# Performance work log

Hardware: AMD Instinct MI355X
Metric: run time of the kernel (lower is better)

Reference implementation:

```python
import jax, jax.numpy as jnp
import numpy as np

N = 80000        # nodes
E = 1280000      # edges
NG = 8           # graphs (segment ids)
F_IN = 3
NC = 20
BN_EPS = 1e-3    # keras BatchNormalization default epsilon


def setup_inputs() -> dict:
    key = jax.random.key(0)
    ks = jax.random.split(key, 16)
    inp = {}
    inp['x'] = jax.random.normal(ks[0], (N, F_IN), dtype=jnp.float32)
    inp['edge_w'] = jax.random.uniform(ks[1], (E,), dtype=jnp.float32)
    inp['src'] = jax.random.randint(ks[2], (E,), 0, N, dtype=jnp.int32)
    inp['dst'] = jax.random.randint(ks[3], (E,), 0, N, dtype=jnp.int32)
    inp['ids'] = jnp.sort(jax.random.randint(ks[4], (N,), 0, NG, dtype=jnp.int32))
    def w(k, fi, fo):
        return jax.random.normal(k, (fi, fo), dtype=jnp.float32) * (1.0 / np.sqrt(fi))
    inp['W1'] = w(ks[5], F_IN, 32); inp['b1'] = jnp.zeros((32,), jnp.float32)
    inp['W2'] = w(ks[6], 32, 32);   inp['b2'] = jnp.zeros((32,), jnp.float32)
    inp['g1'] = jnp.ones((32,), jnp.float32); inp['be1'] = jnp.zeros((32,), jnp.float32)
    inp['m1'] = jax.random.normal(ks[7], (32,), dtype=jnp.float32) * 0.1
    inp['v1'] = jax.random.uniform(ks[8], (32,), dtype=jnp.float32) + 0.5
    inp['W3'] = w(ks[9], 32, 64);   inp['b3'] = jnp.zeros((64,), jnp.float32)
    inp['W4'] = w(ks[10], 64, 64);  inp['b4'] = jnp.zeros((64,), jnp.float32)
    inp['g2'] = jnp.ones((64,), jnp.float32); inp['be2'] = jnp.zeros((64,), jnp.float32)
    inp['m2'] = jax.random.normal(ks[11], (64,), dtype=jnp.float32) * 0.1
    inp['v2'] = jax.random.uniform(ks[12], (64,), dtype=jnp.float32) + 0.5
    inp['W5'] = w(ks[13], 64, NC);  inp['b5'] = jnp.zeros((NC,), jnp.float32)
    return inp


def _gcn(x, W, b, src, dst, ew):
    # Spektral GCNConv: A_norm @ (X W) + b, with A given as edge list (src->dst).
    h = x @ W                                      # [N, Fo] dense transform first (cheaper)
    msg = h[src] * ew[:, None]                     # gather + scale  [E, Fo]
    agg = jax.ops.segment_sum(msg, dst, num_segments=N)  # scatter-add [N, Fo]
    return agg + b


def _bn(x, g, be, m, v):
    # inference-mode BatchNormalization
    return (x - m) * (g * jax.lax.rsqrt(v + BN_EPS)) + be


def _pool(x, ids):
    # per-graph global max pooling, broadcast back to nodes
    mx = jax.ops.segment_max(x, ids, num_segments=NG)   # [NG, F]
    return mx[ids]                                       # [N, F]


def reference(x, edge_w, src, dst, ids,
              W1, b1, W2, b2, g1, be1, m1, v1,
              W3, b3, W4, b4, g2, be2, m2, v2,
              W5, b5):
    h = jax.nn.relu(_gcn(x, W1, b1, src, dst, edge_w))
    h = jax.nn.relu(_gcn(h, W2, b2, src, dst, edge_w))
    h = _bn(h, g1, be1, m1, v1)
    h = _pool(h, ids)
    h = jax.nn.relu(_gcn(h, W3, b3, src, dst, edge_w))
    h = jax.nn.relu(_gcn(h, W4, b4, src, dst, edge_w))
    h = _bn(h, g2, be2, m2, v2)
    h = _pool(h, ids)
    # dropout is identity in inference
    out = jax.nn.softmax(_gcn(h, W5, b5, src, dst, edge_w), axis=-1)
    return out
```

## Files before the change

### kernel.cpp

```cpp
#include <hip/hip_runtime.h>

#define NN 80000
#define NE 1280000
#define NGR 8
#define BN_EPS 1e-3f
#define NBF 625
#define GB 512
#define CHK 2500

typedef unsigned short ushort;
typedef __attribute__((ext_vector_type(8))) short bf16x8;
typedef __attribute__((ext_vector_type(4))) float f32x4;

__device__ __forceinline__ unsigned enc_f(float f) {
    unsigned b = __float_as_uint(f);
    return (f >= 0.f) ? (b | 0x80000000u) : ~b;
}
__device__ __forceinline__ float dec_f(unsigned u) {
    return (u & 0x80000000u) ? __uint_as_float(u & 0x7FFFFFFFu) : __uint_as_float(~u);
}
__device__ __forceinline__ ushort f2bf(float f) {
    unsigned u = __float_as_uint(f);
    unsigned r = u + 0x7FFFu + ((u >> 16) & 1u);
    return (ushort)(r >> 16);
}
__device__ __forceinline__ void fma8(float* acc, const ushort* p, float w) {
    uint4 q = *(const uint4*)p;
    acc[0] += w * __uint_as_float((q.x & 0xFFFFu) << 16);
    acc[1] += w * __uint_as_float(q.x & 0xFFFF0000u);
    acc[2] += w * __uint_as_float((q.y & 0xFFFFu) << 16);
    acc[3] += w * __uint_as_float(q.y & 0xFFFF0000u);
    acc[4] += w * __uint_as_float((q.z & 0xFFFFu) << 16);
    acc[5] += w * __uint_as_float(q.z & 0xFFFF0000u);
    acc[6] += w * __uint_as_float((q.w & 0xFFFFu) << 16);
    acc[7] += w * __uint_as_float(q.w & 0xFFFF0000u);
}

__global__ __launch_bounds__(256) void k_bhist(const int* __restrict__ dst,
                                               int* __restrict__ hcnt) {
    __shared__ int lh[NBF];
    for (int i = threadIdx.x; i < NBF; i += 256) lh[i] = 0;
    __syncthreads();
    int e0 = blockIdx.x * CHK;
    for (int e = e0 + threadIdx.x; e < e0 + CHK; e += 256)
        atomicAdd(&lh[dst[e] >> 7], 1);
    __syncthreads();
    int* row = hcnt + (size_t)blockIdx.x * NBF;
    for (int i = threadIdx.x; i < NBF; i += 256) row[i] = lh[i];
}

__global__ __launch_bounds__(256) void k_bbase1(int* __restrict__ hcnt,
                                                int* __restrict__ tot) {
    __shared__ int sm[256];
    int bin = blockIdx.x, t = threadIdx.x;
    int v[2];
    int s = 0;
    #pragma unroll
    for (int j = 0; j < 2; ++j) {
        v[j] = hcnt[(size_t)(t * 2 + j) * NBF + bin];
        s += v[j];
    }
    sm[t] = s;
    __syncthreads();
    #pragma unroll
    for (int off = 1; off < 256; off <<= 1) {
        int u = (t >= off) ? sm[t - off] : 0;
        __syncthreads();
        sm[t] += u;
        __syncthreads();
    }
    int run = sm[t] - s;
    if (t == 255) tot[bin] = sm[255];
    #pragma unroll
    for (int j = 0; j < 2; ++j) {
        hcnt[(size_t)(t * 2 + j) * NBF + bin] = run;
        run += v[j];
    }
}

__global__ __launch_bounds__(1024) void k_bbase2w(const int* __restrict__ tot,
                                                  int* __restrict__ bo,
                                                  const float* __restrict__ W2,
                                                  const float* __restrict__ W4,
                                                  ushort* __restrict__ W2t,
                                                  ushort* __restrict__ W4t) {
    __shared__ int sm[1024];
    int t = threadIdx.x;
    int v = (t < NBF) ? tot[t] : 0;
    sm[t] = v;
    __syncthreads();
    #pragma unroll
    for (int off = 1; off < 1024; off <<= 1) {
        int u = (t >= off) ? sm[t - off] : 0;
        __syncthreads();
        sm[t] += u;
        __syncthreads();
    }
    if (t < NBF) bo[t] = sm[t] - v;
    if (t == 0) bo[NBF] = NE;
    {
        int f = t >> 5, k = t & 31;
        W2t[t] = f2bf(W2[k * 32 + f]);
    }
    #pragma unroll
    for (int j = 0; j < 4; ++j) {
        int i = t + j * 1024;
        int f = i >> 6, k = i & 63;
        W4t[i] = f2bf(W4[k * 64 + f]);
    }
}

__global__ __launch_bounds__(256) void k_bfill(const int* __restrict__ src,
                                               const int* __restrict__ dst,
                                               const float* __restrict__ ew,
                                               const int* __restrict__ ids,
                                               const int* __restrict__ hcnt,
                                               const int* __restrict__ bo,
                                               int2* __restrict__ cB) {
    __shared__ int lh[NBF];
    __shared__ int delta[NBF];
    __shared__ int lcur[NBF];
    __shared__ int2 srt[CHK];
    __shared__ short sbin[CHK];
    __shared__ int sm[256];
    int t = threadIdx.x;
    int e0 = blockIdx.x * CHK;
    const int* row = hcnt + (size_t)blockIdx.x * NBF;
    for (int i = t; i < NBF; i += 256) lh[i] = 0;
    __syncthreads();
    for (int e = e0 + t; e < e0 + CHK; e += 256)
        atomicAdd(&lh[dst[e] >> 7], 1);
    __syncthreads();
    int c0, c1, c2;
    {
        int i0 = t * 3, i1 = t * 3 + 1, i2 = t * 3 + 2;
        c0 = (i0 < NBF) ? lh[i0] : 0;
        c1 = (i1 < NBF) ? lh[i1] : 0;
        c2 = (i2 < NBF) ? lh[i2] : 0;
    }
    int ssum = c0 + c1 + c2;
    sm[t] = ssum;
    __syncthreads();
    #pragma unroll
    for (int off = 1; off < 256; off <<= 1) {
        int u = (t >= off) ? sm[t - off] : 0;
        __syncthreads();
        sm[t] += u;
        __syncthreads();
    }
    {
        int run = sm[t] - ssum;
        int i0 = t * 3;
        #pragma unroll
        for (int j = 0; j < 3; ++j) {
            int idx = i0 + j;
            int cnt = (j == 0) ? c0 : (j == 1) ? c1 : c2;
            if (idx < NBF) {
                lh[idx] = run;
                delta[idx] = row[idx] + bo[idx] - run;
                lcur[idx] = 0;
            }
            run += cnt;
        }
    }
    __syncthreads();
    for (int e = e0 + t; e < e0 + CHK; e += 256) {
        int d = dst[e];
        int s = src[e];
        int bin = d >> 7;
        int r = atomicAdd(&lcur[bin], 1);
        int slot = lh[bin] + r;
        srt[slot] = make_int2(s | (ids[s] << 17) | ((d & 127) << 20),
                              __float_as_int(ew[e]));
        sbin[slot] = (short)bin;
    }
    __syncthreads();
    for (int p = t; p < CHK; p += 256)
        cB[delta[sbin[p]] + p] = srt[p];
}

__global__ __launch_bounds__(512) void k_insort(const int* __restrict__ bo,
                                                const int2* __restrict__ cB,
                                                const float* __restrict__ x,
                                                int* __restrict__ rp,
                                                int2* __restrict__ cE,
                                                float* __restrict__ S,
                                                float* __restrict__ AX) {
    __shared__ int lc[128];
    __shared__ int loff[128];
    __shared__ int sm[512];
    int bin = blockIdx.x, t = threadIdx.x;
    int s0 = bo[bin], s1 = bo[bin + 1];
    if (t < 128) lc[t] = 0;
    __syncthreads();
    for (int i = s0 + t; i < s1; i += 512)
        atomicAdd(&lc[(cB[i].x >> 20) & 127], 1);
    __syncthreads();
    int v = (t < 128) ? lc[t] : 0;
    sm[t] = v;
    __syncthreads();
    #pragma unroll
    for (int off = 1; off < 128; off <<= 1) {
        int u = (t >= off && t < 128) ? sm[t - off] : 0;
        __syncthreads();
        if (t < 128) sm[t] += u;
        __syncthreads();
    }
    if (t < 128) {
        loff[t] = sm[t] - v;
        rp[bin * 128 + t] = s0 + loff[t];
        lc[t] = 0;
    }
    if (bin == NBF - 1 && t == 0) rp[NN] = NE;
    __syncthreads();
    for (int i = s0 + t; i < s1; i += 512) {
        int2 a = cB[i];
        int dlow = (a.x >> 20) & 127;
        int pos = s0 + loff[dlow] + atomicAdd(&lc[dlow], 1);
        cE[pos] = make_int2((a.x & 0x1FFFF) | (((a.x >> 17) & 7) << 24), a.y);
    }
    __syncthreads();
    int n = t >> 2, q = t & 3;
    int ne0 = s0 + loff[n];
    int ne1 = ne0 + lc[n];
    float sv[8] = {0, 0, 0, 0, 0, 0, 0, 0};
    float ax0 = 0.f, ax1 = 0.f, ax2 = 0.f;
    for (int i = ne0 + q; i < ne1; i += 4) {
        int2 a = cE[i];
        float w = __int_as_float(a.y);
        int s = a.x & 0xFFFFFF;
        int gg = a.x >> 24;
        #pragma unroll
        for (int g = 0; g < 8; ++g) sv[g] += (gg == g) ? w : 0.f;
        const float* xp = x + s * 3;
        ax0 += w * xp[0]; ax1 += w * xp[1]; ax2 += w * xp[2];
    }
    #pragma unroll
    for (int g = 0; g < 8; ++g) {
        sv[g] += __shfl_xor(sv[g], 1);
        sv[g] += __shfl_xor(sv[g], 2);
    }
    ax0 += __shfl_xor(ax0, 1); ax0 += __shfl_xor(ax0, 2);
    ax1 += __shfl_xor(ax1, 1); ax1 += __shfl_xor(ax1, 2);
    ax2 += __shfl_xor(ax2, 1); ax2 += __shfl_xor(ax2, 2);
    if (q == 0) {
        int node = bin * 128 + n;
        float4* Sp = (float4*)(S + (size_t)node * 8);
        Sp[0] = make_float4(sv[0], sv[1], sv[2], sv[3]);
        Sp[1] = make_float4(sv[4], sv[5], sv[6], sv[7]);
        *(float4*)(AX + (size_t)node * 4) = make_float4(ax0, ax1, ax2, 0.f);
    }
}

__global__ __launch_bounds__(256) void k_gpl2(const float* __restrict__ AX,
                                              const float* __restrict__ W1,
                                              const float* __restrict__ b1,
                                              const ushort* __restrict__ W2t,
                                              const int* __restrict__ rp,
                                              const int2* __restrict__ cE,
                                              const int* __restrict__ ids,
                                              const float* __restrict__ b2,
                                              const float* __restrict__ g1,
                                              const float* __restrict__ be1,
                                              const float* __restrict__ m1,
                                              const float* __restrict__ v1,
                                              unsigned* __restrict__ mxe) {
    __shared__ unsigned lmx[NGR * 32];
    __shared__ ushort aggS[64 * 40];
    __shared__ int gids[64];
    int t = threadIdx.x;
    int nb = blockIdx.x * 64;
    lmx[t] = 0u;
    if (t < 64) gids[t] = ids[nb + t];
    int c = t & 3;
    float w1r0[8], w1r1[8], w1r2[8], b1c[8];
    #pragma unroll
    for (int j = 0; j < 8; ++j) {
        int f = c * 8 + j;
        w1r0[j] = W1[f]; w1r1[j] = W1[32 + f]; w1r2[j] = W1[64 + f];
        b1c[j] = b1[f];
    }
    int nl = t >> 2;
    int n = nb + nl;
    int e0 = rp[n], e1 = rp[n + 1];
    float acc[8] = {0, 0, 0, 0, 0, 0, 0, 0};
    for (int i = e0; i < e1; ++i) {
        int2 a = cE[i];
        float w = __int_as_float(a.y);
        float axv = AX[(size_t)(a.x & 0xFFFFFF) * 4 + c];
        float a0 = __shfl(axv, 0, 4);
        float a1 = __shfl(axv, 1, 4);
        float a2 = __shfl(axv, 2, 4);
        #pragma unroll
        for (int j = 0; j < 8; ++j) {
            float pre = b1c[j] + a0 * w1r0[j] + a1 * w1r1[j] + a2 * w1r2[j];
            acc[j] += w * fmaxf(pre, 0.f);
        }
    }
    #pragma unroll
    for (int j = 0; j < 8; ++j) aggS[nl * 40 + c * 8 + j] = f2bf(acc[j]);
    __syncthreads();
    int lane = t & 63, wave = t >> 6;
    int quad = lane >> 4, col = lane & 15;
    bf16x8 afr = *(const bf16x8*)(aggS + (wave * 16 + col) * 40 + quad * 8);
    #pragma unroll
    for (int nt = 0; nt < 2; ++nt) {
        bf16x8 bfr = *(const bf16x8*)(W2t + (nt * 16 + col) * 32 + quad * 8);
        f32x4 d = {0.f, 0.f, 0.f, 0.f};
        d = __builtin_amdgcn_mfma_f32_16x16x32_bf16(afr, bfr, d, 0, 0, 0);
        int f = nt * 16 + col;
        float scale = g1[f] * rsqrtf(v1[f] + BN_EPS);
        float bb = b2[f], mm = m1[f], bee = be1[f];
        #pragma unroll
        for (int r = 0; r < 4; ++r) {
            int node_l = wave * 16 + quad * 4 + r;
            float h = fmaxf(d[r] + bb, 0.f);
            float val = (h - mm) * scale + bee;
            atomicMax(&lmx[gids[node_l] * 32 + f], enc_f(val));
        }
    }
    __syncthreads();
    {
        unsigned u = lmx[t];
        if (u) atomicMax(&mxe[t], u);
    }
}

__global__ __launch_bounds__(256) void k_l34m(const float* __restrict__ S,
                                              const unsigned* __restrict__ mxe,
                                              const float* __restrict__ W3,
                                              const float* __restrict__ b3,
                                              const ushort* __restrict__ W4t,
                                              ushort* __restrict__ T) {
    __shared__ float smxs[256];
    __shared__ float HW3s[512];
    __shared__ ushort h3s[64 * 72];
    int t = threadIdx.x;
    int nb = blockIdx.x * 64;
    smxs[t] = mxe[t] ? dec_f(mxe[t]) : 0.f;
    __syncthreads();
    {
        #pragma unroll
        for (int j = 0; j < 2; ++j) {
            int i = t + j * 256;
            int g = i >> 6, f = i & 63;
            float acc = 0.f;
            #pragma unroll
            for (int k = 0; k < 32; ++k) acc += smxs[g * 32 + k] * W3[k * 64 + f];
            HW3s[i] = acc;
        }
    }
    __syncthreads();
    {
        int f = t & 63, rr = t >> 6;
        float hwc[8];
        #pragma unroll
        for (int g = 0; g < 8; ++g) hwc[g] = HW3s[g * 64 + f];
        float bb = b3[f];
        #pragma unroll
        for (int i = 0; i < 16; ++i) {
            int n = rr + i * 4;
            const float4* sp = (const float4*)(S + (size_t)(nb + n) * 8);
            float4 s0 = sp[0], s1 = sp[1];
            float acc = bb + s0.x * hwc[0] + s0.y * hwc[1] + s0.z * hwc[2] +
                        s0.w * hwc[3] + s1.x * hwc[4] + s1.y * hwc[5] +
                        s1.z * hwc[6] + s1.w * hwc[7];
            h3s[n * 72 + f] = f2bf(fmaxf(acc, 0.f));
        }
    }
    __syncthreads();
    int lane = t & 63, wave = t >> 6;
    int quad = lane >> 4, col = lane & 15;
    int mtile = wave;
    bf16x8 a0 = *(const bf16x8*)(h3s + (mtile * 16 + col) * 72 + quad * 8);
    bf16x8 a1 = *(const bf16x8*)(h3s + (mtile * 16 + col) * 72 + 32 + quad * 8);
    #pragma unroll
    for (int ntile = 0; ntile < 4; ++ntile) {
        bf16x8 b0 = *(const bf16x8*)(W4t + (ntile * 16 + col) * 64 + quad * 8);
        bf16x8 b1v = *(const bf16x8*)(W4t + (ntile * 16 + col) * 64 + 32 + quad * 8);
        f32x4 acc = {0.f, 0.f, 0.f, 0.f};
        acc = __builtin_amdgcn_mfma_f32_16x16x32_bf16(a0, b0, acc, 0, 0, 0);
        acc = __builtin_amdgcn_mfma_f32_16x16x32_bf16(a1, b1v, acc, 0, 0, 0);
        #pragma unroll
        for (int r = 0; r < 4; ++r) {
            int node = nb + mtile * 16 + quad * 4 + r;
            T[node * 64 + ntile * 16 + col] = f2bf(acc[r]);
        }
    }
}

template <int LOGF>
__global__ __launch_bounds__(256) void k_gpool(const ushort* __restrict__ th,
                                               const int* __restrict__ rp,
                                               const int2* __restrict__ cE,
                                               const int* __restrict__ ids,
                                               const float* __restrict__ b,
                                               const float* __restrict__ g,
                                               const float* __restrict__ be,
                                               const float* __restrict__ m,
                                               const float* __restrict__ v,
                                               unsigned* __restrict__ mxe) {
    const int F = 1 << LOGF;
    const int CPN = F >> 3;
    const int NPB = 256 / CPN;
    __shared__ unsigned lmx[NGR * F];
    for (int i = threadIdx.x; i < NGR * F; i += 256) lmx[i] = 0u;
    __syncthreads();
    int c = threadIdx.x & (CPN - 1);
    int n = blockIdx.x * NPB + (threadIdx.x >> (LOGF - 3));
    if (n < NN) {
        int e0 = rp[n], e1 = rp[n + 1];
        float a0[8] = {0, 0, 0, 0, 0, 0, 0, 0};
        float a1[8] = {0, 0, 0, 0, 0, 0, 0, 0};
        float a2[8] = {0, 0, 0, 0, 0, 0, 0, 0};
        float a3[8] = {0, 0, 0, 0, 0, 0, 0, 0};
        int i = e0;
        for (; i + 4 <= e1; i += 4) {
            int2 q0 = cE[i], q1 = cE[i + 1], q2 = cE[i + 2], q3 = cE[i + 3];
            fma8(a0, th + (((size_t)(q0.x & 0xFFFFFF)) << LOGF) + (c << 3), __int_as_float(q0.y));
            fma8(a1, th + (((size_t)(q1.x & 0xFFFFFF)) << LOGF) + (c << 3), __int_as_float(q1.y));
            fma8(a2, th + (((size_t)(q2.x & 0xFFFFFF)) << LOGF) + (c << 3), __int_as_float(q2.y));
            fma8(a3, th + (((size_t)(q3.x & 0xFFFFFF)) << LOGF) + (c << 3), __int_as_float(q3.y));
        }
        for (; i < e1; ++i) {
            int2 q0 = cE[i];
            fma8(a0, th + (((size_t)(q0.x & 0xFFFFFF)) << LOGF) + (c << 3), __int_as_float(q0.y));
        }
        int gg = ids[n];
        #pragma unroll
        for (int j = 0; j < 8; ++j) {
            int f = (c << 3) + j;
            float scale = g[f] * rsqrtf(v[f] + BN_EPS);
            float h = fmaxf((a0[j] + a1[j]) + (a2[j] + a3[j]) + b[f], 0.f);
            float val = (h - m[f]) * scale + be[f];
            atomicMax(&lmx[gg * F + f], enc_f(val));
        }
    }
    __syncthreads();
    for (int i = threadIdx.x; i < NGR * F; i += 256) {
        unsigned u = lmx[i];
        if (u) atomicMax(&mxe[i], u);
    }
}

__global__ __launch_bounds__(256) void k_out(const float* __restrict__ S,
                                             const unsigned* __restrict__ mxe,
                                             const float* __restrict__ W5,
                                             const float* __restrict__ b5,
                                             float* __restrict__ out) {
    __shared__ float smxs[512];
    __shared__ float hw[160];
    __shared__ float bb[20];
    int t = threadIdx.x;
    smxs[t] = mxe[t] ? dec_f(mxe[t]) : 0.f;
    smxs[t + 256] = mxe[t + 256] ? dec_f(mxe[t + 256]) : 0.f;
    if (t < 20) bb[t] = b5[t];
    __syncthreads();
    if (t < 160) {
        int g = t / 20, c = t % 20;
        float acc = 0.f;
        #pragma unroll
        for (int k = 0; k < 64; ++k) acc += smxs[g * 64 + k] * W5[k * 20 + c];
        hw[t] = acc;
    }
    __syncthreads();
    int n = blockIdx.x * 256 + t;
    if (n >= NN) return;
    const float4* sp = (const float4*)(S + (size_t)n * 8);
    float4 s0 = sp[0], s1 = sp[1];
    float sv[8] = {s0.x, s0.y, s0.z, s0.w, s1.x, s1.y, s1.z, s1.w};
    float pre[20];
    #pragma unroll
    for (int c = 0; c < 20; ++c) {
        float acc = bb[c];
        #pragma unroll
        for (int g = 0; g < 8; ++g) acc += sv[g] * hw[g * 20 + c];
        pre[c] = acc;
    }
    float mx = pre[0];
    #pragma unroll
    for (int c = 1; c < 20; ++c) mx = fmaxf(mx, pre[c]);
    float sum = 0.f;
    #pragma unroll
    for (int c = 0; c < 20; ++c) { pre[c] = __expf(pre[c] - mx); sum += pre[c]; }
    float inv = 1.f / sum;
    #pragma unroll
    for (int c = 0; c < 20; ++c) out[n * 20 + c] = pre[c] * inv;
}

extern "C" void kernel_launch(void* const* d_in, const int* in_sizes, int n_in,
                              void* d_out, int out_size, void* d_ws, size_t ws_size,
                              hipStream_t stream) {
    const float* x   = (const float*)d_in[0];
    const float* ew  = (const float*)d_in[1];
    const int*   src = (const int*)d_in[2];
    const int*   dst = (const int*)d_in[3];
    const int*   ids = (const int*)d_in[4];
    const float* W1 = (const float*)d_in[5];  const float* b1 = (const float*)d_in[6];
    const float* W2 = (const float*)d_in[7];  const float* b2 = (const float*)d_in[8];
    const float* g1 = (const float*)d_in[9];  const float* be1 = (const float*)d_in[10];
    const float* m1 = (const float*)d_in[11]; const float* v1 = (const float*)d_in[12];
    const float* W3 = (const float*)d_in[13]; const float* b3 = (const float*)d_in[14];
    const float* W4 = (const float*)d_in[15]; const float* b4 = (const float*)d_in[16];
    const float* g2 = (const float*)d_in[17]; const float* be2 = (const float*)d_in[18];
    const float* m2 = (const float*)d_in[19]; const float* v2 = (const float*)d_in[20];
    const float* W5 = (const float*)d_in[21]; const float* b5 = (const float*)d_in[22];
    float* out = (float*)d_out;

    char* p = (char*)d_ws;
    float*  S    = (float*)p;  p += (size_t)NN * 8 * 4;
    ushort* T    = (ushort*)p; p += (size_t)NN * 64 * 2;
    float*  AX   = (float*)p;  p += (size_t)NN * 4 * 4;
    int*    rp   = (int*)p;    p += (size_t)(NN + 16) * 4;
    int*    hcnt = (int*)p;    p += (size_t)GB * NBF * 4;
    int*    tot  = (int*)p;    p += 1024 * 4;
    int*    bo   = (int*)p;    p += 1024 * 4;
    int2*   cB   = (int2*)p;   p += (size_t)NE * 8;
    int2*   cE   = (int2*)p;   p += (size_t)NE * 8;
    unsigned* MXE1 = (unsigned*)p; p += 256 * 4;
    unsigned* MXE2 = (unsigned*)p; p += 512 * 4;
    ushort* W2t  = (ushort*)p; p += 1024 * 2;
    ushort* W4t  = (ushort*)p; p += 4096 * 2;

    const int BS = 256;
    const int gN = (NN + BS - 1) / BS;

    hipMemsetAsync(MXE1, 0, 768 * 4, stream);
    hipLaunchKernelGGL(k_bhist, dim3(GB), dim3(BS), 0, stream, dst, hcnt);
    hipLaunchKernelGGL(k_bbase1, dim3(NBF), dim3(BS), 0, stream, hcnt, tot);
    hipLaunchKernelGGL(k_bbase2w, dim3(1), dim3(1024), 0, stream, tot, bo, W2, W4, W2t, W4t);
    hipLaunchKernelGGL(k_bfill, dim3(GB), dim3(BS), 0, stream, src, dst, ew, ids, hcnt, bo, cB);
    hipLaunchKernelGGL(k_insort, dim3(NBF), dim3(512), 0, stream, bo, cB, x, rp, cE, S, AX);

    hipLaunchKernelGGL(k_gpl2, dim3(NN / 64), dim3(BS), 0, stream, AX, W1, b1, W2t,
                       rp, cE, ids, b2, g1, be1, m1, v1, MXE1);

    hipLaunchKernelGGL(k_l34m, dim3(NN / 64), dim3(BS), 0, stream, S, MXE1, W3, b3, W4t, T);
    hipLaunchKernelGGL(k_gpool<6>, dim3(NN / 32), dim3(BS), 0, stream, T, rp, cE, ids, b4, g2, be2, m2, v2, MXE2);

    hipLaunchKernelGGL(k_out, dim3(gN), dim3(BS), 0, stream, S, MXE2, W5, b5, out);
}
```

Before: 241.9 us.

## Split layer-4 features into 16-wide slabs and fold scan tail into last block

The layer-4 transformed features T move from one 64-wide bf16 row per node to four 16-wide feature slabs. The gather-pool kernel now loops over the four slabs, keeping two threads per node, so each pass gathers from a smaller, more cache-resident table. Separately, the single-block bin-offset scan, weight transposes and max-buffer clearing are folded into the last block of the per-bin scan kernel using an atomic done counter, which removes one launch and the memset. The trade-off is that each node's edge list is re-read four times in the pool kernel, and the pool kernel now needs more block-wide barriers.

```diff
diff --git a/kernel.cpp b/kernel.cpp
--- a/kernel.cpp
+++ b/kernel.cpp
@@ -49,9 +49,17 @@
     for (int i = threadIdx.x; i < NBF; i += 256) row[i] = lh[i];
 }
 
-__global__ __launch_bounds__(256) void k_bbase1(int* __restrict__ hcnt,
-                                                int* __restrict__ tot) {
+__global__ __launch_bounds__(256) void k_bbase1m(int* __restrict__ hcnt,
+                                                 int* __restrict__ tot,
+                                                 int* __restrict__ done,
+                                                 int* __restrict__ bo,
+                                                 const float* __restrict__ W2,
+                                                 const float* __restrict__ W4,
+                                                 ushort* __restrict__ W2t,
+                                                 ushort* __restrict__ W4t,
+                                                 unsigned* __restrict__ mxe1) {
     __shared__ int sm[256];
+    __shared__ int lastflag;
     int bin = blockIdx.x, t = threadIdx.x;
     int v[2];
     int s = 0;
@@ -76,38 +84,49 @@
         hcnt[(size_t)(t * 2 + j) * NBF + bin] = run;
         run += v[j];
     }
-}
-
-__global__ __launch_bounds__(1024) void k_bbase2w(const int* __restrict__ tot,
-                                                  int* __restrict__ bo,
-                                                  const float* __restrict__ W2,
-                                                  const float* __restrict__ W4,
-                                                  ushort* __restrict__ W2t,
-                                                  ushort* __restrict__ W4t) {
-    __shared__ int sm[1024];
-    int t = threadIdx.x;
-    int v = (t < NBF) ? tot[t] : 0;
-    sm[t] = v;
-    __syncthreads();
-    #pragma unroll
-    for (int off = 1; off < 1024; off <<= 1) {
+    __threadfence();
+    if (t == 0) lastflag = (atomicAdd(done, 1) == NBF - 1) ? 1 : 0;
+    __syncthreads();
+    if (!lastflag) return;
+    __threadfence();
+    int v3[3], ss = 0;
+    #pragma unroll
+    for (int j = 0; j < 3; ++j) {
+        int idx = t * 3 + j;
+        v3[j] = (idx < NBF) ? tot[idx] : 0;
+        ss += v3[j];
+    }
+    __syncthreads();
+    sm[t] = ss;
+    __syncthreads();
+    #pragma unroll
+    for (int off = 1; off < 256; off <<= 1) {
         int u = (t >= off) ? sm[t - off] : 0;
         __syncthreads();
         sm[t] += u;
         __syncthreads();
     }
-    if (t < NBF) bo[t] = sm[t] - v;
+    int run2 = sm[t] - ss;
+    #pragma unroll
+    for (int j = 0; j < 3; ++j) {
+        int idx = t * 3 + j;
+        if (idx < NBF) bo[idx] = run2;
+        run2 += v3[j];
+    }
     if (t == 0) bo[NBF] = NE;
-    {
-        int f = t >> 5, k = t & 31;
-        W2t[t] = f2bf(W2[k * 32 + f]);
-    }
     #pragma unroll
     for (int j = 0; j < 4; ++j) {
-        int i = t + j * 1024;
+        int i = t + j * 256;
+        int f = i >> 5, k = i & 31;
+        W2t[i] = f2bf(W2[k * 32 + f]);
+    }
+    #pragma unroll
+    for (int j = 0; j < 16; ++j) {
+        int i = t + j * 256;
         int f = i >> 6, k = i & 63;
         W4t[i] = f2bf(W4[k * 64 + f]);
     }
+    mxe1[t] = 0u; mxe1[t + 256] = 0u; mxe1[t + 512] = 0u;
 }
 
 __global__ __launch_bounds__(256) void k_bfill(const int* __restrict__ src,
@@ -381,35 +400,35 @@
         f32x4 acc = {0.f, 0.f, 0.f, 0.f};
         acc = __builtin_amdgcn_mfma_f32_16x16x32_bf16(a0, b0, acc, 0, 0, 0);
         acc = __builtin_amdgcn_mfma_f32_16x16x32_bf16(a1, b1v, acc, 0, 0, 0);
+        ushort* Tq = T + (size_t)ntile * NN * 16;
         #pragma unroll
         for (int r = 0; r < 4; ++r) {
             int node = nb + mtile * 16 + quad * 4 + r;
-            T[node * 64 + ntile * 16 + col] = f2bf(acc[r]);
-        }
-    }
-}
-
-template <int LOGF>
-__global__ __launch_bounds__(256) void k_gpool(const ushort* __restrict__ th,
-                                               const int* __restrict__ rp,
-                                               const int2* __restrict__ cE,
-                                               const int* __restrict__ ids,
-                                               const float* __restrict__ b,
-                                               const float* __restrict__ g,
-                                               const float* __restrict__ be,
-                                               const float* __restrict__ m,
-                                               const float* __restrict__ v,
-                                               unsigned* __restrict__ mxe) {
-    const int F = 1 << LOGF;
-    const int CPN = F >> 3;
-    const int NPB = 256 / CPN;
-    __shared__ unsigned lmx[NGR * F];
-    for (int i = threadIdx.x; i < NGR * F; i += 256) lmx[i] = 0u;
-    __syncthreads();
-    int c = threadIdx.x & (CPN - 1);
-    int n = blockIdx.x * NPB + (threadIdx.x >> (LOGF - 3));
-    if (n < NN) {
-        int e0 = rp[n], e1 = rp[n + 1];
+            Tq[(size_t)node * 16 + col] = f2bf(acc[r]);
+        }
+    }
+}
+
+__global__ __launch_bounds__(256) void k_gpool4(const ushort* __restrict__ T,
+                                                const int* __restrict__ rp,
+                                                const int2* __restrict__ cE,
+                                                const int* __restrict__ ids,
+                                                const float* __restrict__ b,
+                                                const float* __restrict__ g,
+                                                const float* __restrict__ be,
+                                                const float* __restrict__ m,
+                                                const float* __restrict__ v,
+                                                unsigned* __restrict__ mxe) {
+    __shared__ unsigned lmx[NGR * 16];
+    int t = threadIdx.x;
+    int c = t & 1, nl = t >> 1;
+    int n = blockIdx.x * 128 + nl;
+    int e0 = rp[n], e1 = rp[n + 1];
+    int gg = ids[n];
+    for (int q = 0; q < 4; ++q) {
+        if (t < 128) lmx[t] = 0u;
+        __syncthreads();
+        const ushort* tq = T + (size_t)q * NN * 16 + (c << 3);
         float a0[8] = {0, 0, 0, 0, 0, 0, 0, 0};
         float a1[8] = {0, 0, 0, 0, 0, 0, 0, 0};
         float a2[8] = {0, 0, 0, 0, 0, 0, 0, 0};
@@ -417,29 +436,30 @@
         int i = e0;
         for (; i + 4 <= e1; i += 4) {
             int2 q0 = cE[i], q1 = cE[i + 1], q2 = cE[i + 2], q3 = cE[i + 3];
-            fma8(a0, th + (((size_t)(q0.x & 0xFFFFFF)) << LOGF) + (c << 3), __int_as_float(q0.y));
-            fma8(a1, th + (((size_t)(q1.x & 0xFFFFFF)) << LOGF) + (c << 3), __int_as_float(q1.y));
-            fma8(a2, th + (((size_t)(q2.x & 0xFFFFFF)) << LOGF) + (c << 3), __int_as_float(q2.y));
-            fma8(a3, th + (((size_t)(q3.x & 0xFFFFFF)) << LOGF) + (c << 3), __int_as_float(q3.y));
+            fma8(a0, tq + ((size_t)(q0.x & 0xFFFFFF) << 4), __int_as_float(q0.y));
+            fma8(a1, tq + ((size_t)(q1.x & 0xFFFFFF) << 4), __int_as_float(q1.y));
+            fma8(a2, tq + ((size_t)(q2.x & 0xFFFFFF) << 4), __int_as_float(q2.y));
+            fma8(a3, tq + ((size_t)(q3.x & 0xFFFFFF) << 4), __int_as_float(q3.y));
         }
         for (; i < e1; ++i) {
             int2 q0 = cE[i];
-            fma8(a0, th + (((size_t)(q0.x & 0xFFFFFF)) << LOGF) + (c << 3), __int_as_float(q0.y));
-        }
-        int gg = ids[n];
+            fma8(a0, tq + ((size_t)(q0.x & 0xFFFFFF) << 4), __int_as_float(q0.y));
+        }
         #pragma unroll
         for (int j = 0; j < 8; ++j) {
-            int f = (c << 3) + j;
+            int fl = (c << 3) + j;
+            int f = (q << 4) + fl;
             float scale = g[f] * rsqrtf(v[f] + BN_EPS);
             float h = fmaxf((a0[j] + a1[j]) + (a2[j] + a3[j]) + b[f], 0.f);
             float val = (h - m[f]) * scale + be[f];
-            atomicMax(&lmx[gg * F + f], enc_f(val));
-        }
-    }
-    __syncthreads();
-    for (int i = threadIdx.x; i < NGR * F; i += 256) {
-        unsigned u = lmx[i];
-        if (u) atomicMax(&mxe[i], u);
+            atomicMax(&lmx[gg * 16 + fl], enc_f(val));
+        }
+        __syncthreads();
+        if (t < 128) {
+            unsigned u = lmx[t];
+            if (u) atomicMax(&mxe[(t >> 4) * 64 + (q << 4) + (t & 15)], u);
+        }
+        __syncthreads();
     }
 }
 
@@ -515,6 +535,7 @@
     int*    hcnt = (int*)p;    p += (size_t)GB * NBF * 4;
     int*    tot  = (int*)p;    p += 1024 * 4;
     int*    bo   = (int*)p;    p += 1024 * 4;
+    int*    done = (int*)p;    p += 256 * 4;
     int2*   cB   = (int2*)p;   p += (size_t)NE * 8;
     int2*   cE   = (int2*)p;   p += (size_t)NE * 8;
     unsigned* MXE1 = (unsigned*)p; p += 256 * 4;
@@ -525,10 +546,10 @@
     const int BS = 256;
     const int gN = (NN + BS - 1) / BS;
 
-    hipMemsetAsync(MXE1, 0, 768 * 4, stream);
+    hipMemsetAsync(done, 0, 4, stream);
     hipLaunchKernelGGL(k_bhist, dim3(GB), dim3(BS), 0, stream, dst, hcnt);
-    hipLaunchKernelGGL(k_bbase1, dim3(NBF), dim3(BS), 0, stream, hcnt, tot);
-    hipLaunchKernelGGL(k_bbase2w, dim3(1), dim3(1024), 0, stream, tot, bo, W2, W4, W2t, W4t);
+    hipLaunchKernelGGL(k_bbase1m, dim3(NBF), dim3(BS), 0, stream, hcnt, tot, done,
+                       bo, W2, W4, W2t, W4t, MXE1);
     hipLaunchKernelGGL(k_bfill, dim3(GB), dim3(BS), 0, stream, src, dst, ew, ids, hcnt, bo, cB);
     hipLaunchKernelGGL(k_insort, dim3(NBF), dim3(512), 0, stream, bo, cB, x, rp, cE, S, AX);
 
@@ -536,7 +557,8 @@
                        rp, cE, ids, b2, g1, be1, m1, v1, MXE1);
 
     hipLaunchKernelGGL(k_l34m, dim3(NN / 64), dim3(BS), 0, stream, S, MXE1, W3, b3, W4t, T);
-    hipLaunchKernelGGL(k_gpool<6>, dim3(NN / 32), dim3(BS), 0, stream, T, rp, cE, ids, b4, g2, be2, m2, v2, MXE2);
+    hipLaunchKernelGGL(k_gpool4, dim3(NN / 128), dim3(BS), 0, stream, T, rp, cE, ids,
+                       b4, g2, be2, m2, v2, MXE2);
 
     hipLaunchKernelGGL(k_out, dim3(gN), dim3(BS), 0, stream, S, MXE2, W5, b5, out);
 }
```

New measurement: 344.2 us. +42.3%, slower.
